# Kernel optimization log

Measured on AMD Instinct MI355X. Metric: run time of the kernel, lower is better.

## Reference

```python
import jax, jax.numpy as jnp
import numpy as np

D_MODEL = 1024
HEADS = 16
HEAD_DIM = D_MODEL // HEADS
EPS = 1e-6


def feature_map(x):
    # F.elu(x) + 1
    return jax.nn.elu(x) + 1.0


def setup_inputs() -> dict:
    key = jax.random.key(0)
    ks = jax.random.split(key, 9)
    B, N, D = 4, 4096, D_MODEL
    s = 1.0 / np.sqrt(D)
    return {
        "x": jax.random.normal(ks[0], (B, N, D), dtype=jnp.float32),
        "Wq": jax.random.normal(ks[1], (D, D), dtype=jnp.float32) * s,
        "bq": jnp.zeros((D,), dtype=jnp.float32),
        "Wk": jax.random.normal(ks[2], (D, D), dtype=jnp.float32) * s,
        "bk": jnp.zeros((D,), dtype=jnp.float32),
        "Wv": jax.random.normal(ks[3], (D, D), dtype=jnp.float32) * s,
        "bv": jnp.zeros((D,), dtype=jnp.float32),
        "Wo": jax.random.normal(ks[4], (D, D), dtype=jnp.float32) * s,
        "bo": jnp.zeros((D,), dtype=jnp.float32),
    }


def reference(x, Wq, bq, Wk, bk, Wv, bv, Wo, bo):
    B, N, D = x.shape
    H, hd = HEADS, HEAD_DIM
    # torch Linear: y = x @ W.T + b
    q = feature_map((x @ Wq.T + bq).reshape(B, N, H, hd))
    k = feature_map((x @ Wk.T + bk).reshape(B, N, H, hd))
    v = (x @ Wv.T + bv).reshape(B, N, H, hd)
    k_sum = k.sum(axis=1)                                   # (B, H, hd)
    D_inv = 1.0 / (jnp.einsum('bnhd,bhd->bnh', q, k_sum) + EPS)
    context = jnp.einsum('bnhd,bnhv->bhdv', k, v)            # (B, H, hd, hd)
    out = jnp.einsum('bnhd,bhdv->bnhv', q, context) * D_inv[..., None]
    out = out.reshape(B, N, D)
    return out @ Wo.T + bo
```

## Files before the change

kernel.cpp:

```cpp
#include <hip/hip_runtime.h>
#include <hip/hip_bf16.h>

typedef __attribute__((ext_vector_type(8))) short bf16x8;
typedef __attribute__((ext_vector_type(4))) float f32x4;

__device__ __forceinline__ float b2f(unsigned short u) {
  union { unsigned int i; float f; } x; x.i = ((unsigned int)u) << 16; return x.f;
}
__device__ __forceinline__ unsigned short f2b(float f) {
  union { __hip_bfloat16 h; unsigned short u; } x; x.h = __float2bfloat16(f); return x.u;
}
__device__ __forceinline__ f32x4 mfma16(bf16x8 a, bf16x8 b, f32x4 c) {
  return __builtin_amdgcn_mfma_f32_16x16x32_bf16(a, b, c, 0, 0, 0);
}
__device__ __forceinline__ void gl16(const void* g, void* l) {
  __builtin_amdgcn_global_load_lds(
      (const __attribute__((address_space(1))) unsigned int*)g,
      (__attribute__((address_space(3))) unsigned int*)l, 16, 0, 0);
}

__global__ __launch_bounds__(256) void cast_k(const float* __restrict__ src,
                                              unsigned short* __restrict__ dst, int n4) {
  int i = blockIdx.x * 256 + threadIdx.x;
  if (i >= n4) return;
  float4 v = ((const float4*)src)[i];
  ushort4 o;
  o.x = f2b(v.x); o.y = f2b(v.y); o.z = f2b(v.z); o.w = f2b(v.w);
  ((ushort4*)dst)[i] = o;
}

__global__ __launch_bounds__(256) void castw_k(
    const float* __restrict__ s0, const float* __restrict__ s1,
    const float* __restrict__ s2, const float* __restrict__ s3,
    unsigned short* __restrict__ d0, unsigned short* __restrict__ d1,
    unsigned short* __restrict__ d2, unsigned short* __restrict__ d3,
    float* __restrict__ ksum) {
  if (blockIdx.x == 4096) {
    ((float4*)ksum)[threadIdx.x * 4 + 0] = make_float4(0.f, 0.f, 0.f, 0.f);
    ((float4*)ksum)[threadIdx.x * 4 + 1] = make_float4(0.f, 0.f, 0.f, 0.f);
    ((float4*)ksum)[threadIdx.x * 4 + 2] = make_float4(0.f, 0.f, 0.f, 0.f);
    ((float4*)ksum)[threadIdx.x * 4 + 3] = make_float4(0.f, 0.f, 0.f, 0.f);
    return;
  }
  int seg = blockIdx.x >> 10;
  int i = (blockIdx.x & 1023) * 256 + threadIdx.x;
  const float* s = (seg == 0) ? s0 : (seg == 1) ? s1 : (seg == 2) ? s2 : s3;
  unsigned short* d = (seg == 0) ? d0 : (seg == 1) ? d1 : (seg == 2) ? d2 : d3;
  float4 v = ((const float4*)s)[i];
  ushort4 o;
  o.x = f2b(v.x); o.y = f2b(v.y); o.z = f2b(v.z); o.w = f2b(v.w);
  ((ushort4*)d)[i] = o;
}

#define BARX() __builtin_amdgcn_s_barrier()
#define LGKM0() asm volatile("s_waitcnt lgkmcnt(0)")
#define WAITV4() asm volatile("s_waitcnt vmcnt(4)")
#define WAITV0() asm volatile("s_waitcnt vmcnt(0)" ::: "memory")
#define P1() __builtin_amdgcn_s_setprio(1)
#define P0() __builtin_amdgcn_s_setprio(0)

#define STAGE_A(BUF, G, TAU) do { \
  gl16(gA_0 + (size_t)(G) * 65536 + (TAU) * 64, sAB + (BUF) * 32768 + (G) * 16384 + u0 * 16); \
  gl16(gA_1 + (size_t)(G) * 65536 + (TAU) * 64, sAB + (BUF) * 32768 + (G) * 16384 + u1 * 16); } while (0)
#define STAGE_B(BUF, G, TAU) do { \
  gl16(gB_0 + (size_t)(G) * 32768 + (TAU) * 64, sAB + 65536 + (BUF) * 32768 + (G) * 16384 + u0 * 16); \
  gl16(gB_1 + (size_t)(G) * 32768 + (TAU) * 64, sAB + 65536 + (BUF) * 32768 + (G) * 16384 + u1 * 16); } while (0)

#define LOAD_A(BUF, MH) do { \
  _Pragma("unroll") for (int mi = 0; mi < 4; ++mi) { \
    const char* p_ = (const char*)sAB + (BUF) * 32768 + (MH) * 16384 + aRd + mi * 2048; \
    af[mi][0] = *(const bf16x8*)(p_ + sr0); \
    af[mi][1] = *(const bf16x8*)(p_ + sr1); } } while (0)
#define LOAD_B(BUF, NH, DST) do { \
  _Pragma("unroll") for (int ni = 0; ni < 2; ++ni) { \
    const char* p_ = (const char*)sAB + 65536 + (BUF) * 32768 + (NH) * 16384 + bRd + ni * 2048; \
    DST[ni][0] = *(const bf16x8*)(p_ + sr0); \
    DST[ni][1] = *(const bf16x8*)(p_ + sr1); } } while (0)

#define QUAD(MH, NH, BF) do { \
  _Pragma("unroll") for (int mi = 0; mi < 4; ++mi) \
    _Pragma("unroll") for (int ni = 0; ni < 2; ++ni) { \
      acc[(MH) * 4 + mi][(NH) * 2 + ni] = mfma16(af[mi][0], BF[ni][0], acc[(MH) * 4 + mi][(NH) * 2 + ni]); \
      acc[(MH) * 4 + mi][(NH) * 2 + ni] = mfma16(af[mi][1], BF[ni][1], acc[(MH) * 4 + mi][(NH) * 2 + ni]); } } while (0)

template<int MODE>
__global__ __launch_bounds__(512, 2) void gemm256(
    const unsigned short* __restrict__ A,
    const unsigned short* __restrict__ W0, const unsigned short* __restrict__ W1,
    const unsigned short* __restrict__ W2,
    const float* __restrict__ bias0, const float* __restrict__ bias1, const float* __restrict__ bias2,
    float* __restrict__ outF,
    unsigned short* __restrict__ o0, unsigned short* __restrict__ o1, unsigned short* __restrict__ o2,
    int tiles_n, float* __restrict__ ksum)
{
  __shared__ char sAB[131072];
  int bid = blockIdx.x;
  int nwg = gridDim.x;
  int cpx = nwg >> 3;
  int sbid = (bid & 7) * cpx + (bid >> 3);
  int tn = sbid % tiles_n, tm = sbid / tiles_n;
  int m0 = tm * 256, n0 = tn * 256;

  const unsigned short* W = W0; const float* bias = bias0; unsigned short* outB = o0;
  int sel = 0;
  if (MODE == 1) {
    sel = n0 >> 10;
    if (sel == 1) { W = W1; bias = bias1; outB = o1; }
    else if (sel == 2) { W = W2; bias = bias2; outB = o2; }
  } else {
    W = W0 + ((size_t)(m0 >> 12) << 20);
  }
  int nloc0 = (MODE == 1) ? (n0 & 1023) : n0;

  int t = threadIdx.x, w = t >> 6, l = t & 63;
  int wm = w >> 2, wn = w & 3;

  int u0 = t, u1 = t + 512;
  int lr0 = u0 >> 3, lr1 = u1 >> 3;
  int sl0 = (u0 & 7) ^ (lr0 & 7), sl1 = (u1 & 7) ^ (lr1 & 7);
  int rA0 = ((lr0 >> 6) << 7) + (lr0 & 63), rA1 = ((lr1 >> 6) << 7) + (lr1 & 63);
  int rB0 = ((lr0 >> 5) << 6) + (lr0 & 31), rB1 = ((lr1 >> 5) << 6) + (lr1 & 31);
  const unsigned short* gA_0 = A + (size_t)(m0 + rA0) * 1024 + sl0 * 8;
  const unsigned short* gA_1 = A + (size_t)(m0 + rA1) * 1024 + sl1 * 8;
  const unsigned short* gB_0 = W + (size_t)(nloc0 + rB0) * 1024 + sl0 * 8;
  const unsigned short* gB_1 = W + (size_t)(nloc0 + rB1) * 1024 + sl1 * 8;

  int aRd = (wm * 64 + (l & 15)) * 128;
  int bRd = (wn * 32 + (l & 15)) * 128;
  int sr0 = (((l >> 4) + 0) ^ (l & 7)) * 16;
  int sr1 = (((l >> 4) + 4) ^ (l & 7)) * 16;

  f32x4 acc[8][4];
  f32x4 zero = {0.f, 0.f, 0.f, 0.f};
#pragma unroll
  for (int i = 0; i < 8; ++i)
#pragma unroll
    for (int jx = 0; jx < 4; ++jx) acc[i][jx] = zero;
  bf16x8 af[4][2], bf0[2][2], bf1[2][2];

  STAGE_A(0, 0, 0); STAGE_B(0, 0, 0); STAGE_A(0, 1, 0); STAGE_B(0, 1, 0);
  STAGE_A(1, 0, 1); STAGE_B(1, 0, 1);
  WAITV4();
  BARX();

  for (int j = 0; j < 8; ++j) {
    int t1 = 2 * j + 1;
    int t2 = (j < 7) ? (2 * j + 2) : 14;
    int t3 = (j < 7) ? (2 * j + 3) : 15;
    LOAD_A(0, 0); LOAD_B(0, 0, bf0);
    STAGE_A(1, 1, t1);
    BARX(); LGKM0(); P1(); QUAD(0, 0, bf0); P0();
    LOAD_B(0, 1, bf1);
    BARX();
    STAGE_B(1, 1, t1);
    BARX(); LGKM0(); P1(); QUAD(0, 1, bf1); P0();
    LOAD_A(0, 1);
    BARX();
    STAGE_A(0, 0, t2);
    BARX(); LGKM0(); P1(); QUAD(1, 0, bf0); P0(); BARX();
    STAGE_B(0, 0, t2);
    BARX(); LGKM0(); P1(); QUAD(1, 1, bf1); P0(); WAITV4(); BARX();
    LOAD_A(1, 0); LOAD_B(1, 0, bf0);
    STAGE_A(0, 1, t2);
    BARX(); LGKM0(); P1(); QUAD(0, 0, bf0); P0();
    LOAD_B(1, 1, bf1);
    BARX();
    STAGE_B(0, 1, t2);
    BARX(); LGKM0(); P1(); QUAD(0, 1, bf1); P0();
    LOAD_A(1, 1);
    BARX();
    STAGE_A(1, 0, t3);
    BARX(); LGKM0(); P1(); QUAD(1, 0, bf0); P0(); BARX();
    STAGE_B(1, 0, t3);
    BARX(); LGKM0(); P1(); QUAD(1, 1, bf1); P0(); WAITV4(); BARX();
  }
  WAITV0();

  if (MODE == 1 && sel >= 1) {
    int b_idx = m0 >> 12;
    int nloc_h = nloc0 >> 6;
#pragma unroll
    for (int mq = 0; mq < 8; ++mq) {
      int r_base = wm * 128 + (mq >> 2) * 64 + (mq & 3) * 16 + ((l >> 4) << 2);
#pragma unroll
      for (int nq = 0; nq < 4; ++nq) {
        int c_loc = wn * 64 + (nq >> 1) * 32 + (nq & 1) * 16 + (l & 15);
        float bb = bias[nloc0 + c_loc];
        float v0 = acc[mq][nq][0] + bb, v1 = acc[mq][nq][1] + bb;
        float v2 = acc[mq][nq][2] + bb, v3 = acc[mq][nq][3] + bb;
        if (sel == 1) {
          v0 = (v0 > 0.0f) ? (v0 + 1.0f) : __expf(v0);
          v1 = (v1 > 0.0f) ? (v1 + 1.0f) : __expf(v1);
          v2 = (v2 > 0.0f) ? (v2 + 1.0f) : __expf(v2);
          v3 = (v3 > 0.0f) ? (v3 + 1.0f) : __expf(v3);
        }
        unsigned long long pk =
            (unsigned long long)(f2b(v0) | ((unsigned int)f2b(v1) << 16)) |
            ((unsigned long long)(f2b(v2) | ((unsigned int)f2b(v3) << 16)) << 32);
        int byte = c_loc * 512 + ((r_base * 2) ^ ((c_loc & 7) << 4));
        *(unsigned long long*)(sAB + byte) = pk;
      }
    }
    __syncthreads();
#pragma unroll
    for (int qq = 0; qq < 16; ++qq) {
      int c_loc = qq * 16 + w * 2 + (l >> 5);
      int n_off = (l & 31) * 8;
      int d = c_loc & 63;
      int bh = b_idx * 16 + nloc_h + (c_loc >> 6);
      int byte = c_loc * 512 + ((n_off * 2) ^ ((c_loc & 7) << 4));
      bf16x8 ch = *(const bf16x8*)(sAB + byte);
      *(bf16x8*)(outB + (size_t)(bh * 64 + d) * 4096 + (m0 & 4095) + n_off) = ch;
      if (sel == 1) {
        float s = 0.f;
#pragma unroll
        for (int jj = 0; jj < 8; ++jj) s += b2f((unsigned short)ch[jj]);
        s += __shfl_xor(s, 1);
        s += __shfl_xor(s, 2);
        s += __shfl_xor(s, 4);
        s += __shfl_xor(s, 8);
        s += __shfl_xor(s, 16);
        if ((l & 31) == 0) atomicAdd(ksum + bh * 64 + d, s);
      }
    }
  } else {
#pragma unroll
    for (int mq = 0; mq < 8; ++mq) {
      int grow = m0 + wm * 128 + (mq >> 2) * 64 + (mq & 3) * 16 + ((l >> 4) << 2);
#pragma unroll
      for (int nq = 0; nq < 4; ++nq) {
        int gcol = n0 + wn * 64 + (nq >> 1) * 32 + (nq & 1) * 16 + (l & 15);
        if (MODE == 0) {
          float bb = bias[gcol];
#pragma unroll
          for (int r = 0; r < 4; ++r)
            outF[(size_t)(grow + r) * 1024 + gcol] = acc[mq][nq][r] + bb;
        } else {
          int c = gcol & 1023;
          float bb = bias[c];
#pragma unroll
          for (int r = 0; r < 4; ++r) {
            float v = acc[mq][nq][r] + bb;
            v = (v > 0.0f) ? (v + 1.0f) : __expf(v);
            outB[(size_t)(grow + r) * 1024 + c] = f2b(v);
          }
        }
      }
    }
  }
}

__global__ __launch_bounds__(256) void ctx_gemm(
    const unsigned short* __restrict__ kT,
    const unsigned short* __restrict__ vT,
    float* __restrict__ ctxP)
{
  __shared__ float red[4][64 * 65];
  int bid = blockIdx.x;
  int bh = bid >> 3, ch = bid & 7;
  int t = threadIdx.x, wv = t >> 6, l = t & 63;
  int noff = ch * 512 + wv * 128 + ((l >> 4) << 3);
  const unsigned short* aB = kT + ((size_t)bh * 64 + (l & 15)) * 4096 + noff;
  const unsigned short* bB = vT + ((size_t)bh * 64 + (l & 15)) * 4096 + noff;
  f32x4 acc[4][4];
  f32x4 zero = {0.f, 0.f, 0.f, 0.f};
#pragma unroll
  for (int i = 0; i < 4; ++i)
#pragma unroll
    for (int j = 0; j < 4; ++j) acc[i][j] = zero;
  for (int ks = 0; ks < 4; ++ks) {
    bf16x8 av[4], bv[4];
#pragma unroll
    for (int mi = 0; mi < 4; ++mi) av[mi] = *(const bf16x8*)(aB + (size_t)mi * 16 * 4096 + ks * 32);
#pragma unroll
    for (int ni = 0; ni < 4; ++ni) bv[ni] = *(const bf16x8*)(bB + (size_t)ni * 16 * 4096 + ks * 32);
#pragma unroll
    for (int mi = 0; mi < 4; ++mi)
#pragma unroll
      for (int ni = 0; ni < 4; ++ni)
        acc[mi][ni] = mfma16(av[mi], bv[ni], acc[mi][ni]);
  }
#pragma unroll
  for (int mi = 0; mi < 4; ++mi)
#pragma unroll
    for (int ni = 0; ni < 4; ++ni)
#pragma unroll
      for (int r = 0; r < 4; ++r) {
        int dd = mi * 16 + ((l >> 4) << 2) + r;
        int vv = ni * 16 + (l & 15);
        red[wv][dd * 65 + vv] = acc[mi][ni][r];
      }
  __syncthreads();
  for (int o = t; o < 4096; o += 256) {
    int idx = (o >> 6) * 65 + (o & 63);
    ctxP[(size_t)bid * 4096 + o] = red[0][idx] + red[1][idx] + red[2][idx] + red[3][idx];
  }
}

__global__ __launch_bounds__(1024) void ctxwo_k(
    const float* __restrict__ ctxP,
    const unsigned short* __restrict__ wo,
    unsigned short* __restrict__ M)
{
  __shared__ float cs[4096];
  int bh = blockIdx.x;
  int b = bh >> 4, h = bh & 15;
  int t = threadIdx.x, wv = t >> 6, l = t & 63;
  int j0 = wv * 64;

  for (int o = t; o < 4096; o += 1024) {
    float s = 0.f;
#pragma unroll
    for (int ch = 0; ch < 8; ++ch) s += ctxP[((size_t)bh * 8 + ch) * 4096 + o];
    cs[o] = s;
  }
  __syncthreads();

  bf16x8 af[4][2], bf[4][2];
#pragma unroll
  for (int mi = 0; mi < 4; ++mi)
#pragma unroll
    for (int ks = 0; ks < 2; ++ks)
      af[mi][ks] = *(const bf16x8*)(wo + (size_t)(j0 + mi * 16 + (l & 15)) * 1024 +
                                    h * 64 + ((l >> 4) << 3) + ks * 32);
#pragma unroll
  for (int ni = 0; ni < 4; ++ni)
#pragma unroll
    for (int ks = 0; ks < 2; ++ks) {
      const float* p = cs + (ni * 16 + (l & 15)) * 64 + ((l >> 4) << 3) + ks * 32;
#pragma unroll
      for (int jj = 0; jj < 8; ++jj) bf[ni][ks][jj] = (short)f2b(p[jj]);
    }

  f32x4 acc[4][4];
  f32x4 zero = {0.f, 0.f, 0.f, 0.f};
#pragma unroll
  for (int i = 0; i < 4; ++i)
#pragma unroll
    for (int j = 0; j < 4; ++j) acc[i][j] = zero;
#pragma unroll
  for (int mi = 0; mi < 4; ++mi)
#pragma unroll
    for (int ni = 0; ni < 4; ++ni) {
      acc[mi][ni] = mfma16(af[mi][0], bf[ni][0], acc[mi][ni]);
      acc[mi][ni] = mfma16(af[mi][1], bf[ni][1], acc[mi][ni]);
    }

  unsigned short* Mb = M + ((size_t)b << 20);
#pragma unroll
  for (int mi = 0; mi < 4; ++mi)
#pragma unroll
    for (int ni = 0; ni < 4; ++ni)
#pragma unroll
      for (int r = 0; r < 4; ++r) {
        int j = j0 + mi * 16 + ((l >> 4) << 2) + r;
        int d = ni * 16 + (l & 15);
        Mb[(size_t)j * 1024 + h * 64 + d] = f2b(acc[mi][ni][r]);
      }
}

__global__ __launch_bounds__(256) void dinvq_k(
    unsigned short* __restrict__ q,
    const float* __restrict__ ksum)
{
  int t = threadIdx.x, wv = t >> 6, l = t & 63;
  int n = blockIdx.x * 4 + wv;
  int b = n >> 12;
  int h = l >> 2;
  unsigned short* qp = q + (size_t)n * 1024 + l * 16;
  const float* kp = ksum + (b * 16 + h) * 64 + (l & 3) * 16;
  bf16x8 v0 = *(const bf16x8*)qp;
  bf16x8 v1 = *(const bf16x8*)(qp + 8);
  float s = 0.f;
#pragma unroll
  for (int j = 0; j < 8; ++j) {
    s += b2f((unsigned short)v0[j]) * kp[j];
    s += b2f((unsigned short)v1[j]) * kp[8 + j];
  }
  s += __shfl_xor(s, 1);
  s += __shfl_xor(s, 2);
  float di = 1.0f / (s + 1e-6f);
#pragma unroll
  for (int j = 0; j < 8; ++j) {
    v0[j] = (short)f2b(b2f((unsigned short)v0[j]) * di);
    v1[j] = (short)f2b(b2f((unsigned short)v1[j]) * di);
  }
  *(bf16x8*)qp = v0;
  *(bf16x8*)(qp + 8) = v1;
}

extern "C" void kernel_launch(void* const* d_in, const int* in_sizes, int n_in,
                              void* d_out, int out_size, void* d_ws, size_t ws_size,
                              hipStream_t stream)
{
  const float* x  = (const float*)d_in[0];
  const float* bq = (const float*)d_in[2];
  const float* bk = (const float*)d_in[4];
  const float* bv = (const float*)d_in[6];
  const float* bo = (const float*)d_in[8];
  const float* Wq = (const float*)d_in[1];
  const float* Wk = (const float*)d_in[3];
  const float* Wv = (const float*)d_in[5];
  const float* Wo = (const float*)d_in[7];
  float* out = (float*)d_out;

  char* ws = (char*)d_ws;
  const size_t SB = (size_t)16384 * 1024 * 2;
  const size_t NEED = 4 * SB + 4 * (1u << 21) + 2 * (1u << 20) + (1u << 14);
  if (ws_size < NEED) return;

  unsigned short* xb  = (unsigned short*)(ws);
  unsigned short* qb  = (unsigned short*)(ws + SB);
  unsigned short* kTb = (unsigned short*)(ws + 2 * SB);
  unsigned short* vTb = (unsigned short*)(ws + 3 * SB);
  unsigned short* wqb = (unsigned short*)(ws + 4 * SB);
  unsigned short* wkb = (unsigned short*)(ws + 4 * SB + (1u << 21));
  unsigned short* wvb = (unsigned short*)(ws + 4 * SB + (2u << 21));
  unsigned short* wob = (unsigned short*)(ws + 4 * SB + (3u << 21));
  float* ksum = (float*)(ws + 4 * SB + (4u << 21) + (2u << 20));
  unsigned short* Mbuf = xb;
  float* ctxP = (float*)(ws + (8u << 20));

  cast_k<<<16384, 256, 0, stream>>>(x, xb, 16777216 / 4);
  castw_k<<<4097, 256, 0, stream>>>(Wq, Wk, Wv, Wo, wqb, wkb, wvb, wob, ksum);

  gemm256<1><<<768, 512, 0, stream>>>(xb, wqb, wkb, wvb, bq, bk, bv,
                                      nullptr, qb, kTb, vTb, 12, ksum);

  ctx_gemm<<<512, 256, 0, stream>>>(kTb, vTb, ctxP);

  ctxwo_k<<<64, 1024, 0, stream>>>(ctxP, wob, Mbuf);

  dinvq_k<<<4096, 256, 0, stream>>>(qb, ksum);

  gemm256<0><<<256, 512, 0, stream>>>(qb, Mbuf, nullptr, nullptr, bo, nullptr, nullptr,
                                      out, nullptr, nullptr, nullptr, 4, nullptr);
}
```

Baseline: 219.9 us.

## Merge cast and dinv kernels into neighbors and drop redundant GEMM barriers

Folds the x cast and the weight casts into a single launch, and folds the D_inv scaling of q into the context GEMM launch as extra blocks. This removes two kernel launches and their gaps. It also removes the barrier that preceded each MFMA quad in the main GEMM loop, and adds one barrier after the loop before the epilogue. Dropping those barriers cuts sync stalls, but it risks LDS races if a wave reads a stage buffer before other waves have finished filling it.

```diff
diff --git a/kernel.cpp b/kernel.cpp
--- a/kernel.cpp
+++ b/kernel.cpp
@@ -19,37 +19,37 @@
       (__attribute__((address_space(3))) unsigned int*)l, 16, 0, 0);
 }
 
-__global__ __launch_bounds__(256) void cast_k(const float* __restrict__ src,
-                                              unsigned short* __restrict__ dst, int n4) {
-  int i = blockIdx.x * 256 + threadIdx.x;
-  if (i >= n4) return;
-  float4 v = ((const float4*)src)[i];
-  ushort4 o;
-  o.x = f2b(v.x); o.y = f2b(v.y); o.z = f2b(v.z); o.w = f2b(v.w);
-  ((ushort4*)dst)[i] = o;
-}
-
-__global__ __launch_bounds__(256) void castw_k(
+__global__ __launch_bounds__(256) void cast_all(
+    const float* __restrict__ x,
     const float* __restrict__ s0, const float* __restrict__ s1,
     const float* __restrict__ s2, const float* __restrict__ s3,
+    unsigned short* __restrict__ xb,
     unsigned short* __restrict__ d0, unsigned short* __restrict__ d1,
     unsigned short* __restrict__ d2, unsigned short* __restrict__ d3,
     float* __restrict__ ksum) {
-  if (blockIdx.x == 4096) {
+  int bid = blockIdx.x;
+  if (bid < 16384) {
+    int i = bid * 256 + threadIdx.x;
+    float4 v = ((const float4*)x)[i];
+    ushort4 o;
+    o.x = f2b(v.x); o.y = f2b(v.y); o.z = f2b(v.z); o.w = f2b(v.w);
+    ((ushort4*)xb)[i] = o;
+  } else if (bid < 20480) {
+    int r = bid - 16384;
+    int seg = r >> 10;
+    int i = (r & 1023) * 256 + threadIdx.x;
+    const float* s = (seg == 0) ? s0 : (seg == 1) ? s1 : (seg == 2) ? s2 : s3;
+    unsigned short* d = (seg == 0) ? d0 : (seg == 1) ? d1 : (seg == 2) ? d2 : d3;
+    float4 v = ((const float4*)s)[i];
+    ushort4 o;
+    o.x = f2b(v.x); o.y = f2b(v.y); o.z = f2b(v.z); o.w = f2b(v.w);
+    ((ushort4*)d)[i] = o;
+  } else {
     ((float4*)ksum)[threadIdx.x * 4 + 0] = make_float4(0.f, 0.f, 0.f, 0.f);
     ((float4*)ksum)[threadIdx.x * 4 + 1] = make_float4(0.f, 0.f, 0.f, 0.f);
     ((float4*)ksum)[threadIdx.x * 4 + 2] = make_float4(0.f, 0.f, 0.f, 0.f);
     ((float4*)ksum)[threadIdx.x * 4 + 3] = make_float4(0.f, 0.f, 0.f, 0.f);
-    return;
-  }
-  int seg = blockIdx.x >> 10;
-  int i = (blockIdx.x & 1023) * 256 + threadIdx.x;
-  const float* s = (seg == 0) ? s0 : (seg == 1) ? s1 : (seg == 2) ? s2 : s3;
-  unsigned short* d = (seg == 0) ? d0 : (seg == 1) ? d1 : (seg == 2) ? d2 : d3;
-  float4 v = ((const float4*)s)[i];
-  ushort4 o;
-  o.x = f2b(v.x); o.y = f2b(v.y); o.z = f2b(v.z); o.w = f2b(v.w);
-  ((ushort4*)d)[i] = o;
+  }
 }
 
 #define BARX() __builtin_amdgcn_s_barrier()
@@ -149,32 +149,33 @@
     int t3 = (j < 7) ? (2 * j + 3) : 15;
     LOAD_A(0, 0); LOAD_B(0, 0, bf0);
     STAGE_A(1, 1, t1);
-    BARX(); LGKM0(); P1(); QUAD(0, 0, bf0); P0();
+    LGKM0(); P1(); QUAD(0, 0, bf0); P0();
     LOAD_B(0, 1, bf1);
     BARX();
     STAGE_B(1, 1, t1);
-    BARX(); LGKM0(); P1(); QUAD(0, 1, bf1); P0();
+    LGKM0(); P1(); QUAD(0, 1, bf1); P0();
     LOAD_A(0, 1);
     BARX();
     STAGE_A(0, 0, t2);
-    BARX(); LGKM0(); P1(); QUAD(1, 0, bf0); P0(); BARX();
+    LGKM0(); P1(); QUAD(1, 0, bf0); P0(); BARX();
     STAGE_B(0, 0, t2);
-    BARX(); LGKM0(); P1(); QUAD(1, 1, bf1); P0(); WAITV4(); BARX();
+    LGKM0(); P1(); QUAD(1, 1, bf1); P0(); WAITV4(); BARX();
     LOAD_A(1, 0); LOAD_B(1, 0, bf0);
     STAGE_A(0, 1, t2);
-    BARX(); LGKM0(); P1(); QUAD(0, 0, bf0); P0();
+    LGKM0(); P1(); QUAD(0, 0, bf0); P0();
     LOAD_B(1, 1, bf1);
     BARX();
     STAGE_B(0, 1, t2);
-    BARX(); LGKM0(); P1(); QUAD(0, 1, bf1); P0();
+    LGKM0(); P1(); QUAD(0, 1, bf1); P0();
     LOAD_A(1, 1);
     BARX();
     STAGE_A(1, 0, t3);
-    BARX(); LGKM0(); P1(); QUAD(1, 0, bf0); P0(); BARX();
+    LGKM0(); P1(); QUAD(1, 0, bf0); P0(); BARX();
     STAGE_B(1, 0, t3);
-    BARX(); LGKM0(); P1(); QUAD(1, 1, bf1); P0(); WAITV4(); BARX();
+    LGKM0(); P1(); QUAD(1, 1, bf1); P0(); WAITV4(); BARX();
   }
   WAITV0();
+  BARX();
 
   if (MODE == 1 && sel >= 1) {
     int b_idx = m0 >> 12;
@@ -250,15 +251,43 @@
   }
 }
 
-__global__ __launch_bounds__(256) void ctx_gemm(
+__global__ __launch_bounds__(256) void ctx_dinv_k(
     const unsigned short* __restrict__ kT,
     const unsigned short* __restrict__ vT,
-    float* __restrict__ ctxP)
+    float* __restrict__ ctxP,
+    unsigned short* __restrict__ q,
+    const float* __restrict__ ksum)
 {
   __shared__ float red[4][64 * 65];
   int bid = blockIdx.x;
+  int t = threadIdx.x, wv = t >> 6, l = t & 63;
+  if (bid >= 512) {
+    int n = (bid - 512) * 4 + wv;
+    int b = n >> 12;
+    int h = l >> 2;
+    unsigned short* qp = q + (size_t)n * 1024 + l * 16;
+    const float* kp = ksum + (b * 16 + h) * 64 + (l & 3) * 16;
+    bf16x8 v0 = *(const bf16x8*)qp;
+    bf16x8 v1 = *(const bf16x8*)(qp + 8);
+    float s = 0.f;
+#pragma unroll
+    for (int j = 0; j < 8; ++j) {
+      s += b2f((unsigned short)v0[j]) * kp[j];
+      s += b2f((unsigned short)v1[j]) * kp[8 + j];
+    }
+    s += __shfl_xor(s, 1);
+    s += __shfl_xor(s, 2);
+    float di = 1.0f / (s + 1e-6f);
+#pragma unroll
+    for (int j = 0; j < 8; ++j) {
+      v0[j] = (short)f2b(b2f((unsigned short)v0[j]) * di);
+      v1[j] = (short)f2b(b2f((unsigned short)v1[j]) * di);
+    }
+    *(bf16x8*)qp = v0;
+    *(bf16x8*)(qp + 8) = v1;
+    return;
+  }
   int bh = bid >> 3, ch = bid & 7;
-  int t = threadIdx.x, wv = t >> 6, l = t & 63;
   int noff = ch * 512 + wv * 128 + ((l >> 4) << 3);
   const unsigned short* aB = kT + ((size_t)bh * 64 + (l & 15)) * 4096 + noff;
   const unsigned short* bB = vT + ((size_t)bh * 64 + (l & 15)) * 4096 + noff;
@@ -357,36 +386,6 @@
         int d = ni * 16 + (l & 15);
         Mb[(size_t)j * 1024 + h * 64 + d] = f2b(acc[mi][ni][r]);
       }
-}
-
-__global__ __launch_bounds__(256) void dinvq_k(
-    unsigned short* __restrict__ q,
-    const float* __restrict__ ksum)
-{
-  int t = threadIdx.x, wv = t >> 6, l = t & 63;
-  int n = blockIdx.x * 4 + wv;
-  int b = n >> 12;
-  int h = l >> 2;
-  unsigned short* qp = q + (size_t)n * 1024 + l * 16;
-  const float* kp = ksum + (b * 16 + h) * 64 + (l & 3) * 16;
-  bf16x8 v0 = *(const bf16x8*)qp;
-  bf16x8 v1 = *(const bf16x8*)(qp + 8);
-  float s = 0.f;
-#pragma unroll
-  for (int j = 0; j < 8; ++j) {
-    s += b2f((unsigned short)v0[j]) * kp[j];
-    s += b2f((unsigned short)v1[j]) * kp[8 + j];
-  }
-  s += __shfl_xor(s, 1);
-  s += __shfl_xor(s, 2);
-  float di = 1.0f / (s + 1e-6f);
-#pragma unroll
-  for (int j = 0; j < 8; ++j) {
-    v0[j] = (short)f2b(b2f((unsigned short)v0[j]) * di);
-    v1[j] = (short)f2b(b2f((unsigned short)v1[j]) * di);
-  }
-  *(bf16x8*)qp = v0;
-  *(bf16x8*)(qp + 8) = v1;
 }
 
 extern "C" void kernel_launch(void* const* d_in, const int* in_sizes, int n_in,
@@ -421,17 +420,14 @@
   unsigned short* Mbuf = xb;
   float* ctxP = (float*)(ws + (8u << 20));
 
-  cast_k<<<16384, 256, 0, stream>>>(x, xb, 16777216 / 4);
-  castw_k<<<4097, 256, 0, stream>>>(Wq, Wk, Wv, Wo, wqb, wkb, wvb, wob, ksum);
+  cast_all<<<20481, 256, 0, stream>>>(x, Wq, Wk, Wv, Wo, xb, wqb, wkb, wvb, wob, ksum);
 
   gemm256<1><<<768, 512, 0, stream>>>(xb, wqb, wkb, wvb, bq, bk, bv,
                                       nullptr, qb, kTb, vTb, 12, ksum);
 
-  ctx_gemm<<<512, 256, 0, stream>>>(kTb, vTb, ctxP);
+  ctx_dinv_k<<<4608, 256, 0, stream>>>(kTb, vTb, ctxP, qb, ksum);
 
   ctxwo_k<<<64, 1024, 0, stream>>>(ctxP, wob, Mbuf);
-
-  dinvq_k<<<4096, 256, 0, stream>>>(qb, ksum);
 
   gemm256<0><<<256, 512, 0, stream>>>(qb, Mbuf, nullptr, nullptr, bo, nullptr, nullptr,
                                       out, nullptr, nullptr, nullptr, 4, nullptr);
```

Result: faster. 214.3 us (median of 2 runs) (-2.6%).
